# Performance work log

Hardware: AMD Instinct MI355X
Metric: run time of the kernel (lower is better)

## Reference

```python
import jax, jax.numpy as jnp
import numpy as np

BN_EPS = 1e-5

def setup_inputs() -> dict:
    key = jax.random.key(0)
    ks = jax.random.split(key, 8)
    B, N, d_in, d_out, M, K = 16, 16384, 64, 128, 4096, 16
    pos = jax.random.normal(ks[0], (B, N, 3), dtype=jnp.float32)
    feat = jax.random.normal(ks[1], (B, N, d_in), dtype=jnp.float32)
    fps_preprocess = jax.random.randint(ks[2], (B, M), 0, N, dtype=jnp.int64)
    k_idx = jax.random.randint(ks[3], (B, M, K), 0, N, dtype=jnp.int64)
    W = jax.random.normal(ks[4], (d_out, d_in), dtype=jnp.float32) / np.sqrt(d_in)
    b = jax.random.normal(ks[5], (d_out,), dtype=jnp.float32) * 0.01
    gamma = jnp.ones((d_out,), dtype=jnp.float32)
    beta = jnp.zeros((d_out,), dtype=jnp.float32)
    return {"pos": pos, "feat": feat, "fps_preprocess": fps_preprocess,
            "k_idx": k_idx, "W": W, "b": b, "gamma": gamma, "beta": beta}

def reference(pos, feat, fps_preprocess, k_idx, W, b, gamma, beta):
    B = pos.shape[0]
    # Linear: [B,N,d_in] @ [d_in,d_out] -> [B,N,d_out]
    h = jnp.einsum('bnd,od->bno', feat, W) + b
    # BatchNorm1d over channels (batch stats, biased variance) + ReLU
    mu = jnp.mean(h, axis=(0, 1))
    var = jnp.mean(jnp.square(h - mu), axis=(0, 1))
    h = jax.nn.relu(gamma * (h - mu) * jax.lax.rsqrt(var + BN_EPS) + beta)
    # Downsample positions via FPS indices: [B,M,3]
    pos_ds = jnp.take_along_axis(pos, fps_preprocess[:, :, None], axis=1)
    # Batched kNN gather [B,M,K,d_out] then max over neighbors
    bidx = jnp.arange(B)[:, None, None]
    feat_knn = h[bidx, k_idx]            # [B,M,K,d_out]
    feat_ds = jnp.max(feat_knn, axis=2)  # [B,M,d_out]
    return (pos_ds, feat_ds)
```

## Files before the change

kernel.cpp:

```cpp
#include <hip/hip_runtime.h>
#include <hip/hip_bf16.h>
#include <stdint.h>

typedef float f4 __attribute__((ext_vector_type(4)));
typedef float f32x4v __attribute__((ext_vector_type(4)));
typedef float f32x16 __attribute__((ext_vector_type(16)));
typedef short bf16x8 __attribute__((ext_vector_type(8)));
typedef unsigned int u32x2 __attribute__((ext_vector_type(2)));

static constexpr int Bc = 16, Nc = 16384, DIN = 64, DOUT = 128, Mc = 4096, KNN = 16;
static constexpr long Rr = (long)Bc * Nc;
static constexpr float EPS = 1e-5f;
static constexpr int POS_OUT = Bc * Mc * 3;
static constexpr int GBLK = 512;
static constexpr int PSTRIDE = 4160;
static constexpr int RGRP = 32;
static constexpr int CG_STRIDE = 8224;

__device__ __forceinline__ uint32_t cvt2(float a, float b) {
    union { __hip_bfloat162 h; uint32_t u; } c;
    c.h = __float22bfloat162_rn(make_float2(a, b));
    return c.u;
}

__global__ __launch_bounds__(256) void k_gram(const float* __restrict__ feat,
                                              unsigned short* __restrict__ feat16,
                                              float* __restrict__ part)
{
    __shared__ alignas(16) char lds[4 * CG_STRIDE];
    const int t = threadIdx.x;
    const int lane = t & 63;
    const int w = t >> 6;
    const long R0 = (long)blockIdx.x * 512;
    const f4* feat4 = (const f4*)feat;
    const unsigned lds_base = (unsigned)(size_t)&lds[0];

    f32x4v acc[4][4];
#pragma unroll
    for (int mi = 0; mi < 4; ++mi)
#pragma unroll
        for (int mj = 0; mj < 4; ++mj) acc[mi][mj] = (f32x4v){0.f, 0.f, 0.f, 0.f};
    f4 csum = (f4){0.f, 0.f, 0.f, 0.f};

    f4 v[16];
#pragma unroll
    for (int i = 0; i < 16; ++i)
        v[i] = feat4[R0 * 16 + t + i * 256];

    const int c4 = t & 15;
    const int cg = c4 >> 2;

    for (int ch = 0; ch < 2; ++ch) {
#pragma unroll
        for (int i = 0; i < 16; ++i) {
            int row = (t + i * 256) >> 4;
            uint2 pk = {cvt2(v[i][0], v[i][1]), cvt2(v[i][2], v[i][3])};
            csum += v[i];
            *(uint2*)(feat16 + (size_t)(R0 + ch * 256 + row) * 64 + c4 * 4) = pk;
            *(uint2*)(lds + cg * CG_STRIDE + row * 32 + (c4 & 3) * 8) = pk;
        }
        __syncthreads();
        if (ch == 0) {
#pragma unroll
            for (int i = 0; i < 16; ++i)
                v[i] = feat4[(R0 + 256) * 16 + t + i * 256];
        }
#pragma unroll
        for (int s = 0; s < 2; ++s) {
            const unsigned base = lds_base + (unsigned)((w * 2 + s) * 32 * 32 + lane * 8);
            u32x2 r0[4], r1[4];
#pragma unroll
            for (int g = 0; g < 4; ++g) {
                unsigned a = base + g * CG_STRIDE;
                asm volatile("ds_read_b64_tr_b16 %0, %2 offset:0\n\t"
                             "ds_read_b64_tr_b16 %1, %2 offset:512"
                             : "=v"(r0[g]), "=v"(r1[g]) : "v"(a));
            }
            asm volatile("s_waitcnt lgkmcnt(0)" ::: "memory");
            __builtin_amdgcn_sched_barrier(0);
            bf16x8 f[4];
#pragma unroll
            for (int g = 0; g < 4; ++g) {
                union { u32x2 p[2]; bf16x8 v8; } u;
                u.p[0] = r0[g]; u.p[1] = r1[g];
                f[g] = u.v8;
            }
#pragma unroll
            for (int mi = 0; mi < 4; ++mi)
#pragma unroll
                for (int mj = 0; mj < 4; ++mj)
                    acc[mi][mj] = __builtin_amdgcn_mfma_f32_16x16x32_bf16(
                        f[mi], f[mj], acc[mi][mj], 0, 0, 0);
        }
        __syncthreads();
    }

    float* fbuf = (float*)lds;
    ((f4*)fbuf)[t] = csum;
    __syncthreads();
    float* pb = part + (size_t)blockIdx.x * PSTRIDE;
    if (t < 16) {
        f4 s = (f4){0.f, 0.f, 0.f, 0.f};
#pragma unroll
        for (int q = 0; q < 16; ++q) s += ((f4*)fbuf)[q * 16 + t];
        ((f4*)pb)[t] = s;
    }
    __syncthreads();
    float* buf = fbuf + (w & 1) * 4096;
    const int lcol = lane & 15, lrow4 = (lane >> 4) * 4;
    if (w < 2) {
#pragma unroll
        for (int mi = 0; mi < 4; ++mi)
#pragma unroll
            for (int mj = 0; mj < 4; ++mj)
#pragma unroll
                for (int rg = 0; rg < 4; ++rg)
                    buf[(mi * 16 + lrow4 + rg) * 64 + mj * 16 + lcol] = acc[mi][mj][rg];
    }
    __syncthreads();
    if (w >= 2) {
#pragma unroll
        for (int mi = 0; mi < 4; ++mi)
#pragma unroll
            for (int mj = 0; mj < 4; ++mj)
#pragma unroll
                for (int rg = 0; rg < 4; ++rg)
                    buf[(mi * 16 + lrow4 + rg) * 64 + mj * 16 + lcol] += acc[mi][mj][rg];
    }
    __syncthreads();
#pragma unroll
    for (int q = 0; q < 16; ++q) {
        int e = t + q * 256;
        pb[64 + e] = fbuf[e] + fbuf[4096 + e];
    }
}

__global__ __launch_bounds__(256) void k_reduce1(const float* __restrict__ part,
                                                 float* __restrict__ part2)
{
    const int gid = blockIdx.x * 256 + threadIdx.x;
    const int grp = blockIdx.y;
    if (gid >= PSTRIDE) return;
    const float* pp = part + (size_t)grp * (GBLK / RGRP) * PSTRIDE + gid;
    float s[8];
#pragma unroll
    for (int j = 0; j < 8; ++j) s[j] = 0.f;
#pragma unroll
    for (int i = 0; i < GBLK / RGRP; i += 8)
#pragma unroll
        for (int j = 0; j < 8; ++j)
            s[j] += pp[(size_t)(i + j) * PSTRIDE];
    part2[(size_t)grp * PSTRIDE + gid] =
        ((s[0] + s[1]) + (s[2] + s[3])) + ((s[4] + s[5]) + (s[6] + s[7]));
}

__global__ __launch_bounds__(256) void k_reduce2(const float* __restrict__ part2,
                                                 float* __restrict__ stats)
{
    const int gid = blockIdx.x * 256 + threadIdx.x;
    if (gid >= PSTRIDE) return;
    float s[8];
#pragma unroll
    for (int j = 0; j < 8; ++j) s[j] = 0.f;
#pragma unroll
    for (int i = 0; i < RGRP; i += 8)
#pragma unroll
        for (int j = 0; j < 8; ++j)
            s[j] += part2[(size_t)(i + j) * PSTRIDE + gid];
    stats[gid] = ((s[0] + s[1]) + (s[2] + s[3])) + ((s[4] + s[5]) + (s[6] + s[7]));
}

__global__ __launch_bounds__(256) void k_gram_at(const float* __restrict__ feat,
                                                 float* __restrict__ stats)
{
    __shared__ float tile[64 * 64];
    f4* tile4 = (f4*)tile;
    const f4* feat4 = (const f4*)feat;
    const int t = threadIdx.x;
    const int i0 = (t >> 4) << 2;
    const int j0 = (t & 15) << 2;
    float acc[16];
#pragma unroll
    for (int k = 0; k < 16; ++k) acc[k] = 0.f;
    float csum = 0.f;
    for (int c = 0; c < 8; ++c) {
        const int base4 = (blockIdx.x * 512 + c * 64) * 16;
        __syncthreads();
#pragma unroll
        for (int k = 0; k < 4; ++k) tile4[t + k * 256] = feat4[base4 + t + k * 256];
        __syncthreads();
        for (int r = 0; r < 64; ++r) {
            f4 fi = tile4[r * 16 + (i0 >> 2)];
            f4 fj = tile4[r * 16 + (j0 >> 2)];
#pragma unroll
            for (int ii = 0; ii < 4; ++ii)
#pragma unroll
                for (int jj = 0; jj < 4; ++jj)
                    acc[ii * 4 + jj] = fmaf(fi[ii], fj[jj], acc[ii * 4 + jj]);
        }
        if (t < 64) {
            for (int r = 0; r < 64; ++r) csum += tile[r * 64 + t];
        }
    }
#pragma unroll
    for (int ii = 0; ii < 4; ++ii)
#pragma unroll
        for (int jj = 0; jj < 4; ++jj)
            atomicAdd(&stats[64 + (i0 + ii) * 64 + (j0 + jj)], acc[ii * 4 + jj]);
    if (t < 64) atomicAdd(&stats[t], csum);
}

__global__ __launch_bounds__(64) void k_stats(const float* __restrict__ stats,
                                              const float* __restrict__ W,
                                              const float* __restrict__ gamma,
                                              const float* __restrict__ beta,
                                              float* __restrict__ ST)
{
    const int o = blockIdx.x;
    const int i = threadIdx.x;
    __shared__ float wrow[64];
    wrow[i] = W[o * 64 + i];
    __syncthreads();
    const float* G = stats + 64;
    float inner = 0.f;
    for (int j = 0; j < 64; ++j) inner = fmaf(G[i * 64 + j], wrow[j], inner);
    float qi = inner * wrow[i];
    float cwi = stats[i] * wrow[i];
#pragma unroll
    for (int off = 32; off > 0; off >>= 1) {
        qi += __shfl_down(qi, off);
        cwi += __shfl_down(cwi, off);
    }
    if (i == 0) {
        const double invR = 1.0 / (double)Rr;
        double meanr = (double)cwi * invR;
        double var = (double)qi * invR - meanr * meanr;
        float s = gamma[o] / sqrtf((float)var + EPS);
        ST[o] = s;
        ST[DOUT + o] = beta[o] - (float)meanr * s;
    }
}

__global__ __launch_bounds__(512) void k_gmax(const unsigned short* __restrict__ feat16,
                                              const float* __restrict__ W,
                                              const float* __restrict__ ST,
                                              const int* __restrict__ kidx,
                                              const int* __restrict__ fps,
                                              const float* __restrict__ pos,
                                              float* __restrict__ out)
{
    __shared__ char lW[16 * 1024];
    const int t = threadIdx.x;
    const f4* W4 = (const f4*)W;
#pragma unroll
    for (int i = 0; i < 4; ++i) {
        int idx = t + i * 512;
        int row = idx >> 4, c4 = idx & 15;
        f4 v = W4[idx];
        uint2 pk = {cvt2(v[0], v[1]), cvt2(v[2], v[3])};
        *(uint2*)(lW + row * 128 + ((c4 * 8) ^ ((row & 7) << 4))) = pk;
    }

    const int lane = t & 63;
    const int w = t >> 6;
    const int l31 = lane & 31;
    const int hi = lane >> 5;

    const int bl = blockIdx.x;
    const int jj = bl >> 3;
    const int batch = (bl & 7) + 8 * (jj >> 6);
    const int base = batch * Mc + (jj & 63) * 64 + w * 8;

    int ids[2][2];
#pragma unroll
    for (int i = 0; i < 2; ++i)
#pragma unroll
        for (int it = 0; it < 2; ++it)
            ids[i][it] = __builtin_nontemporal_load(&kidx[(base + i * 4 + 2 * it) * KNN + l31]);

    __syncthreads();

    const unsigned short* fb = feat16 + (size_t)batch * Nc * 64 + hi * 8;

#pragma unroll
    for (int i = 0; i < 2; ++i) {
        const int p0 = base + i * 4;

        bf16x8 A[2][4];
#pragma unroll
        for (int it = 0; it < 2; ++it) {
            const unsigned short* rp = fb + (size_t)ids[i][it] * 64;
            A[it][0] = *(const bf16x8*)(rp);
            A[it][1] = *(const bf16x8*)(rp + 16);
            A[it][2] = *(const bf16x8*)(rp + 32);
            A[it][3] = *(const bf16x8*)(rp + 48);
        }

        if (l31 < 3) {
#pragma unroll
            for (int it = 0; it < 2; ++it) {
                int p = p0 + 2 * it + hi;
                int id2 = fps[p];
                __builtin_nontemporal_store(pos[((size_t)batch * Nc + id2) * 3 + l31],
                                            &out[p * 3 + l31]);
            }
        }

#pragma unroll
        for (int cgh = 0; cgh < 2; ++cgh) {
            bf16x8 wf[2][4];
#pragma unroll
            for (int cc = 0; cc < 2; ++cc) {
                int row = cgh * 64 + cc * 32 + l31;
#pragma unroll
                for (int ks = 0; ks < 4; ++ks)
                    wf[cc][ks] = *(const bf16x8*)(lW + row * 128 +
                                                  ((ks * 32 + hi * 16) ^ ((row & 7) << 4)));
            }
#pragma unroll
            for (int it = 0; it < 2; ++it) {
#pragma unroll
                for (int cc = 0; cc < 2; ++cc) {
                    const int cg = cgh * 2 + cc;
                    f32x16 acc = {};
                    __builtin_amdgcn_s_setprio(1);
#pragma unroll
                    for (int ks = 0; ks < 4; ++ks)
                        acc = __builtin_amdgcn_mfma_f32_32x32x16_bf16(A[it][ks], wf[cc][ks], acc, 0, 0, 0);
                    __builtin_amdgcn_s_setprio(0);
                    float vmA = fmaxf(fmaxf(fmaxf(acc[0], acc[1]), fmaxf(acc[2], acc[3])),
                                      fmaxf(fmaxf(acc[4], acc[5]), fmaxf(acc[6], acc[7])));
                    float vmB = fmaxf(fmaxf(fmaxf(acc[8], acc[9]), fmaxf(acc[10], acc[11])),
                                      fmaxf(fmaxf(acc[12], acc[13]), fmaxf(acc[14], acc[15])));
                    vmA = fmaxf(vmA, __shfl_xor(vmA, 32));
                    vmB = fmaxf(vmB, __shfl_xor(vmB, 32));
                    float vsel = hi ? vmB : vmA;
                    float sc = ST[cg * 32 + l31];
                    float tc = ST[DOUT + cg * 32 + l31];
                    __builtin_nontemporal_store(
                        fmaxf(fmaf(vsel, sc, tc), 0.f),
                        &out[POS_OUT + (size_t)(p0 + 2 * it + hi) * DOUT + cg * 32 + l31]);
                }
            }
        }
    }
}

__global__ __launch_bounds__(128) void k_gather_rc(const float* __restrict__ feat,
                                                   const float* __restrict__ W,
                                                   const float* __restrict__ ST,
                                                   const int* __restrict__ kidx,
                                                   const int* __restrict__ fps,
                                                   const float* __restrict__ pos,
                                                   float* __restrict__ out)
{
    __shared__ float frow[KNN][DIN];
    const int p = blockIdx.x;
    const int o = threadIdx.x;
    const int b = p >> 12;
    const f4* featf = (const f4*)feat;
    f4* frow4 = (f4*)frow;
#pragma unroll
    for (int q = 0; q < 2; ++q) {
        int jj = o + q * 128;
        int row = jj >> 4, i4 = jj & 15;
        int id = kidx[p * KNN + row];
        frow4[jj] = featf[((size_t)b * Nc + id) * 16 + i4];
    }
    __syncthreads();
    float wreg[64];
#pragma unroll
    for (int i4 = 0; i4 < 16; ++i4) {
        f4 wv = ((const f4*)W)[o * 16 + i4];
        wreg[i4 * 4 + 0] = wv[0];
        wreg[i4 * 4 + 1] = wv[1];
        wreg[i4 * 4 + 2] = wv[2];
        wreg[i4 * 4 + 3] = wv[3];
    }
    const float s = ST[o], tt = ST[DOUT + o];
    float vm = 0.f;
    for (int k = 0; k < KNN; ++k) {
        float acc = 0.f;
#pragma unroll
        for (int i = 0; i < 64; ++i) acc = fmaf(frow[k][i], wreg[i], acc);
        vm = fmaxf(vm, fmaf(acc, s, tt));
    }
    out[POS_OUT + (size_t)p * DOUT + o] = vm;
    if (o < 3) {
        int id = fps[p];
        out[p * 3 + o] = pos[((size_t)b * Nc + id) * 3 + o];
    }
}

extern "C" void kernel_launch(void* const* d_in, const int* in_sizes, int n_in,
                              void* d_out, int out_size, void* d_ws, size_t ws_size,
                              hipStream_t stream)
{
    const float* pos   = (const float*)d_in[0];
    const float* feat  = (const float*)d_in[1];
    const int*   fps   = (const int*)d_in[2];
    const int*   kidx  = (const int*)d_in[3];
    const float* W     = (const float*)d_in[4];
    const float* gamma = (const float*)d_in[6];
    const float* beta  = (const float*)d_in[7];
    float* out = (float*)d_out;

    float* stats = (float*)d_ws;
    float* ST = stats + PSTRIDE;
    const size_t F16_OFF = 32768;
    const size_t F16_BYTES = (size_t)Rr * DIN * 2;
    unsigned short* feat16 = (unsigned short*)((char*)d_ws + F16_OFF);
    float* part  = (float*)((char*)d_ws + F16_OFF + F16_BYTES);
    float* part2 = part + (size_t)GBLK * PSTRIDE;
    const size_t need = F16_OFF + F16_BYTES +
                        (size_t)(GBLK + RGRP) * PSTRIDE * 4;

    if (ws_size >= need) {
        k_gram<<<GBLK, 256, 0, stream>>>(feat, feat16, part);
        k_reduce1<<<dim3((PSTRIDE + 255) / 256, RGRP), 256, 0, stream>>>(part, part2);
        k_reduce2<<<(PSTRIDE + 255) / 256, 256, 0, stream>>>(part2, stats);
        k_stats<<<DOUT, 64, 0, stream>>>(stats, W, gamma, beta, ST);
        k_gmax<<<1024, 512, 0, stream>>>(feat16, W, ST, kidx, fps, pos, out);
    } else {
        hipMemsetAsync(d_ws, 0, PSTRIDE * 4, stream);
        k_gram_at<<<512, 256, 0, stream>>>(feat, stats);
        k_stats<<<DOUT, 64, 0, stream>>>(stats, W, gamma, beta, ST);
        k_gather_rc<<<Bc * Mc, 128, 0, stream>>>(feat, W, ST, kidx, fps, pos, out);
    }
}
```

Measured before the change: 66.39 us.

## Stage gathered rows through LDS with coalesced loads in a persistent-grid gmax kernel

The gather-max kernel becomes a persistent loop over a 768-block grid. Each block strides through work chunks and prefetches the next chunk's neighbor indices. Gathered bf16 feature rows are now fetched by 8 lanes per row as 16-byte vectors, which improves coalescing. The rows are written to a swizzled per-wave LDS buffer and then read back as MFMA operands. The BN scale and shift are hoisted into registers. The change adds 32KB of LDS per block and an extra LDS round trip, and each wave now handles fewer points per iteration, which may reduce occupancy and instruction-level parallelism.

```diff
diff --git a/kernel.cpp b/kernel.cpp
--- a/kernel.cpp
+++ b/kernel.cpp
@@ -250,6 +250,7 @@
                                               float* __restrict__ out)
 {
     __shared__ char lW[16 * 1024];
+    __shared__ char lA[8][4096];
     const int t = threadIdx.x;
     const f4* W4 = (const f4*)W;
 #pragma unroll
@@ -265,83 +266,85 @@
     const int w = t >> 6;
     const int l31 = lane & 31;
     const int hi = lane >> 5;
-
-    const int bl = blockIdx.x;
-    const int jj = bl >> 3;
-    const int batch = (bl & 7) + 8 * (jj >> 6);
-    const int base = batch * Mc + (jj & 63) * 64 + w * 8;
-
-    int ids[2][2];
-#pragma unroll
-    for (int i = 0; i < 2; ++i)
-#pragma unroll
-        for (int it = 0; it < 2; ++it)
-            ids[i][it] = __builtin_nontemporal_load(&kidx[(base + i * 4 + 2 * it) * KNN + l31]);
-
-    __syncthreads();
-
-    const unsigned short* fb = feat16 + (size_t)batch * Nc * 64 + hi * 8;
-
-#pragma unroll
-    for (int i = 0; i < 2; ++i) {
-        const int p0 = base + i * 4;
-
-        bf16x8 A[2][4];
-#pragma unroll
-        for (int it = 0; it < 2; ++it) {
-            const unsigned short* rp = fb + (size_t)ids[i][it] * 64;
-            A[it][0] = *(const bf16x8*)(rp);
-            A[it][1] = *(const bf16x8*)(rp + 16);
-            A[it][2] = *(const bf16x8*)(rp + 32);
-            A[it][3] = *(const bf16x8*)(rp + 48);
+    const int lg = lane >> 3;
+    const int lc = lane & 7;
+
+    const int x = blockIdx.x & 7;
+    const int k0 = blockIdx.x >> 3;
+
+    char* myA = lA[w];
+
+    float sc[4], tc[4];
+#pragma unroll
+    for (int cg = 0; cg < 4; ++cg) {
+        sc[cg] = ST[cg * 32 + l31];
+        tc[cg] = ST[DOUT + cg * 32 + l31];
+    }
+
+    int batch = x + 8 * (k0 >> 8);
+    int p0n = batch * Mc + (k0 & 255) * 16 + w * 2;
+    int idsn = __builtin_nontemporal_load(&kidx[p0n * KNN + l31]);
+
+    __syncthreads();
+
+    for (int cc = k0; cc < 512; cc += 96) {
+        const int batchc = x + 8 * (cc >> 8);
+        const char* fbp = (const char*)feat16 + (size_t)batchc * Nc * 128;
+        const int p0 = p0n;
+        const int ids = idsn;
+        if (cc + 96 < 512) {
+            int b2 = x + 8 * ((cc + 96) >> 8);
+            p0n = b2 * Mc + ((cc + 96) & 255) * 16 + w * 2;
+            idsn = __builtin_nontemporal_load(&kidx[p0n * KNN + l31]);
+        }
+
+        f4 g[4];
+#pragma unroll
+        for (int i2 = 0; i2 < 4; ++i2) {
+            int rid = __shfl(ids, i2 * 8 + lg);
+            g[i2] = *(const f4*)(fbp + (size_t)rid * 128 + lc * 16);
+        }
+#pragma unroll
+        for (int i2 = 0; i2 < 4; ++i2) {
+            int rsrc = i2 * 8 + lg;
+            *(f4*)(myA + rsrc * 128 + ((lc * 16) ^ ((rsrc & 7) << 4))) = g[i2];
         }
 
         if (l31 < 3) {
-#pragma unroll
-            for (int it = 0; it < 2; ++it) {
-                int p = p0 + 2 * it + hi;
-                int id2 = fps[p];
-                __builtin_nontemporal_store(pos[((size_t)batch * Nc + id2) * 3 + l31],
-                                            &out[p * 3 + l31]);
+            int p = p0 + hi;
+            int id2 = fps[p];
+            __builtin_nontemporal_store(pos[((size_t)batchc * Nc + id2) * 3 + l31],
+                                        &out[p * 3 + l31]);
+        }
+
+        bf16x8 A[4];
+#pragma unroll
+        for (int ks = 0; ks < 4; ++ks)
+            A[ks] = *(const bf16x8*)(myA + l31 * 128 +
+                                     ((hi * 16 + ks * 32) ^ ((l31 & 7) << 4)));
+
+#pragma unroll
+        for (int cg = 0; cg < 4; ++cg) {
+            const int row = cg * 32 + l31;
+            f32x16 acc = {};
+            __builtin_amdgcn_s_setprio(1);
+#pragma unroll
+            for (int ks = 0; ks < 4; ++ks) {
+                bf16x8 wfv = *(const bf16x8*)(lW + row * 128 +
+                                              ((ks * 32 + hi * 16) ^ ((row & 7) << 4)));
+                acc = __builtin_amdgcn_mfma_f32_32x32x16_bf16(A[ks], wfv, acc, 0, 0, 0);
             }
-        }
-
-#pragma unroll
-        for (int cgh = 0; cgh < 2; ++cgh) {
-            bf16x8 wf[2][4];
-#pragma unroll
-            for (int cc = 0; cc < 2; ++cc) {
-                int row = cgh * 64 + cc * 32 + l31;
-#pragma unroll
-                for (int ks = 0; ks < 4; ++ks)
-                    wf[cc][ks] = *(const bf16x8*)(lW + row * 128 +
-                                                  ((ks * 32 + hi * 16) ^ ((row & 7) << 4)));
-            }
-#pragma unroll
-            for (int it = 0; it < 2; ++it) {
-#pragma unroll
-                for (int cc = 0; cc < 2; ++cc) {
-                    const int cg = cgh * 2 + cc;
-                    f32x16 acc = {};
-                    __builtin_amdgcn_s_setprio(1);
-#pragma unroll
-                    for (int ks = 0; ks < 4; ++ks)
-                        acc = __builtin_amdgcn_mfma_f32_32x32x16_bf16(A[it][ks], wf[cc][ks], acc, 0, 0, 0);
-                    __builtin_amdgcn_s_setprio(0);
-                    float vmA = fmaxf(fmaxf(fmaxf(acc[0], acc[1]), fmaxf(acc[2], acc[3])),
-                                      fmaxf(fmaxf(acc[4], acc[5]), fmaxf(acc[6], acc[7])));
-                    float vmB = fmaxf(fmaxf(fmaxf(acc[8], acc[9]), fmaxf(acc[10], acc[11])),
-                                      fmaxf(fmaxf(acc[12], acc[13]), fmaxf(acc[14], acc[15])));
-                    vmA = fmaxf(vmA, __shfl_xor(vmA, 32));
-                    vmB = fmaxf(vmB, __shfl_xor(vmB, 32));
-                    float vsel = hi ? vmB : vmA;
-                    float sc = ST[cg * 32 + l31];
-                    float tc = ST[DOUT + cg * 32 + l31];
-                    __builtin_nontemporal_store(
-                        fmaxf(fmaf(vsel, sc, tc), 0.f),
-                        &out[POS_OUT + (size_t)(p0 + 2 * it + hi) * DOUT + cg * 32 + l31]);
-                }
-            }
+            __builtin_amdgcn_s_setprio(0);
+            float vmA = fmaxf(fmaxf(fmaxf(acc[0], acc[1]), fmaxf(acc[2], acc[3])),
+                              fmaxf(fmaxf(acc[4], acc[5]), fmaxf(acc[6], acc[7])));
+            float vmB = fmaxf(fmaxf(fmaxf(acc[8], acc[9]), fmaxf(acc[10], acc[11])),
+                              fmaxf(fmaxf(acc[12], acc[13]), fmaxf(acc[14], acc[15])));
+            vmA = fmaxf(vmA, __shfl_xor(vmA, 32));
+            vmB = fmaxf(vmB, __shfl_xor(vmB, 32));
+            float vsel = hi ? vmB : vmA;
+            __builtin_nontemporal_store(
+                fmaxf(fmaf(vsel, sc[cg], tc[cg]), 0.f),
+                &out[POS_OUT + (size_t)(p0 + hi) * DOUT + cg * 32 + l31]);
         }
     }
 }
@@ -420,7 +423,7 @@
         k_reduce1<<<dim3((PSTRIDE + 255) / 256, RGRP), 256, 0, stream>>>(part, part2);
         k_reduce2<<<(PSTRIDE + 255) / 256, 256, 0, stream>>>(part2, stats);
         k_stats<<<DOUT, 64, 0, stream>>>(stats, W, gamma, beta, ST);
-        k_gmax<<<1024, 512, 0, stream>>>(feat16, W, ST, kidx, fps, pos, out);
+        k_gmax<<<768, 512, 0, stream>>>(feat16, W, ST, kidx, fps, pos, out);
     } else {
         hipMemsetAsync(d_ws, 0, PSTRIDE * 4, stream);
         k_gram_at<<<512, 256, 0, stream>>>(feat, stats);
```

Measured after the change: 66.62 us. No clear change (+0.4%).
